# Kernel tuning notes

Measured on AMD Instinct MI355X. Metric: run time of the kernel, lower is better.

Reference implementation:

```python
import jax, jax.numpy as jnp
import numpy as np

B, C_IN, C_OUT, H, W, K, NK = 16, 256, 256, 64, 64, 3, 2
EPS = 1e-8


def setup_inputs() -> dict:
    key = jax.random.key(0)
    k1, k2, k3, k4 = jax.random.split(key, 4)
    x = jax.random.normal(k1, (B, C_IN, H, W), dtype=jnp.float32)
    mod = jax.random.normal(k2, (B, C_IN), dtype=jnp.float32)
    kernel_mod = jax.random.normal(k3, (B, NK), dtype=jnp.float32)
    # kernel bank: [num_conv_kernels, dim_out, dim_in, k, k] (kaiming-ish scale)
    weights = jax.random.normal(k4, (NK, C_OUT, C_IN, K, K), dtype=jnp.float32) / np.sqrt(C_IN * K * K)
    gamma = jnp.ones((C_OUT,), dtype=jnp.float32)
    return {"x": x, "mod": mod, "kernel_mod": kernel_mod, "weights": weights, "gamma": gamma}


def _block(x, mod, kernel_mod, weights, gamma):
    # adaptive kernel selection: softmax-mix the kernel bank per sample
    attn = jax.nn.softmax(kernel_mod, axis=-1)                       # [b, n]
    w = jnp.einsum('bn,noikl->boikl', attn, weights)                 # [b, o, i, k, k]
    # style modulation over input channels
    w = w * (mod[:, None, :, None, None] + 1.0)
    # demodulation
    denom = jnp.clip(jnp.sum(w * w, axis=(2, 3, 4), keepdims=True), EPS)
    w = w * jax.lax.rsqrt(denom)
    # per-sample conv (groups=b trick in torch) -> vmap over batch
    def conv_one(fmap, wb):
        return jax.lax.conv_general_dilated(
            fmap[None], wb, window_strides=(1, 1), padding='SAME',
            dimension_numbers=('NCHW', 'OIHW', 'NCHW'))[0]
    y = jax.vmap(conv_one)(x, w)                                     # [b, o, h, w]
    # RMSNorm over channel dim: F.normalize(x, dim=1) * gamma * sqrt(dim)
    norm = jnp.sqrt(jnp.sum(y * y, axis=1, keepdims=True))
    y = y / jnp.maximum(norm, 1e-12)
    y = y * gamma[None, :, None, None] * (gamma.shape[0] ** 0.5)
    # SiLU
    return y * jax.nn.sigmoid(y)


def reference(x, mod, kernel_mod, weights, gamma):
    return _block(x, mod, kernel_mod, weights, gamma)
```

## Files before the change

kernel.cpp:

```cpp
#include <hip/hip_runtime.h>
#include <math.h>


typedef __attribute__((ext_vector_type(8))) short short8;
typedef __attribute__((ext_vector_type(16))) float f32x16;

#define GLL16(src, dst)                                                       \
  __builtin_amdgcn_global_load_lds(                                           \
      (const __attribute__((address_space(1))) unsigned int*)(src),           \
      (__attribute__((address_space(3))) unsigned int*)(dst), 16, 0, 0)

static __device__ __forceinline__ unsigned short f2bf(float v) {
  union { float f; unsigned u; } u;
  u.f = v;
  unsigned r = u.u + 0x7FFF + ((u.u >> 16) & 1);
  return (unsigned short)(r >> 16);
}

__global__ __launch_bounds__(256) void wprep(
    const float* __restrict__ mod, const float* __restrict__ kmod,
    const float* __restrict__ weights, unsigned short* __restrict__ wq) {
  int blk = blockIdx.x;
  int b = blk >> 5, oq = blk & 31;
  int t = threadIdx.x;
  int o_l = t >> 5, its = t & 31;
  int o = oq * 8 + o_l;

  float k0 = kmod[b * 2 + 0], k1 = kmod[b * 2 + 1];
  float mx = fmaxf(k0, k1);
  float e0 = expf(k0 - mx), e1 = expf(k1 - mx);
  float ai = 1.0f / (e0 + e1);
  float a0 = e0 * ai, a1 = e1 * ai;

  float wv[9][8];
  float s = 0.0f;
  const float* w0 = &weights[((size_t)o * 256 + its * 8) * 9];
  const float* w1 = w0 + 589824;
#pragma unroll
  for (int e = 0; e < 8; ++e) {
    float f = mod[b * 256 + its * 8 + e] + 1.0f;
#pragma unroll
    for (int j = 0; j < 9; ++j) {
      float v = (a0 * w0[e * 9 + j] + a1 * w1[e * 9 + j]) * f;
      wv[j][e] = v;
      s = fmaf(v, v, s);
    }
  }

  __shared__ float red[8][32];
  __shared__ float scl[8];
  red[o_l][its] = s;
  __syncthreads();
  if (t < 8) {
    float tot = 0.0f;
#pragma unroll
    for (int k = 0; k < 32; ++k) tot += red[t][k];
    scl[t] = rsqrtf(fmaxf(tot, 1e-8f));
  }
  __syncthreads();
  float sc = scl[o_l];

  int c = its >> 1, io = its & 1;
  int oh = o >> 7, mf = (o >> 5) & 3;
  int lane2 = (o & 31) + io * 32;
  size_t cbase = ((size_t)(b * 16 + c)) * 36864 + oh * 2048 + mf * 512 + lane2 * 8;
#pragma unroll
  for (int j = 0; j < 9; ++j) {
    short8 pk;
#pragma unroll
    for (int e = 0; e < 8; ++e) pk[e] = (short)f2bf(wv[j][e] * sc);
    *(short8*)(wq + cbase + j * 4096) = pk;
  }
}

__global__ __launch_bounds__(256) void xprep(
    const float* __restrict__ x, unsigned short* __restrict__ xq) {
  int blk = blockIdx.x;
  int rowp = blk % 66;
  int bc = blk / 66;
  int b = bc >> 4, c = bc & 15;
  int t = threadIdx.x;
  size_t obase = (size_t)blk * 1056;

  if (rowp == 0 || rowp == 65) {
    for (int idx = t; idx < 1056; idx += 256) xq[obase + idx] = 0;
    return;
  }
  __shared__ __align__(16) unsigned short xs2[1056];
  int row = rowp - 1;
  for (int idx = t; idx < 1056; idx += 256) xs2[idx] = 0;
  __syncthreads();
#pragma unroll
  for (int k = 0; k < 4; ++k) {
    int idx = t + k * 256;
    int il = idx >> 6, col = idx & 63;
    float v = x[(((size_t)b * 256 + c * 16 + il) * 64 + row) * 64 + col];
    xs2[(col + 1) * 16 + il] = f2bf(v);
  }
  __syncthreads();
  if (t < 132) *(short8*)(xq + obase + (size_t)t * 8) = *(const short8*)&xs2[t * 8];
}

__global__ __launch_bounds__(512, 2) void conv_fused(
    const unsigned short* __restrict__ xq, const unsigned short* __restrict__ wq,
    const float* __restrict__ gamma, float* __restrict__ out) {
  __shared__ __align__(16) unsigned short xsm[2][8192];
  __shared__ float redl[1024];
  __shared__ float invs[256];
  __shared__ float gsm[256];

  int bid = blockIdx.x;
  int xcd = bid & 7;
  int kk = bid >> 3;
  int b = xcd * 2 + (kk >> 4);
  int rt = kk & 15;
  int r0 = rt * 4;

  int t = threadIdx.x;
  int w = t >> 6, lane = t & 63;
  int oh = w & 1, ps = w >> 1;
  int l31 = lane & 31, l5 = lane >> 5;

  if (t < 256) gsm[t] = gamma[t];

  int boffs[9];
#pragma unroll
  for (int T = 0; T < 9; ++T) {
    int kh = T / 3, kw = T % 3;
    boffs[T] = (ps + kh) * 2112 + (l31 + kw) * 32 + l5 * 16;
  }

  f32x16 acc[4][2];
#pragma unroll
  for (int mf = 0; mf < 4; ++mf)
#pragma unroll
    for (int h = 0; h < 2; ++h)
#pragma unroll
      for (int q = 0; q < 16; ++q) acc[mf][h][q] = 0.f;

#define GLLX(cn, nb)                                                           \
  _Pragma("unroll") for (int r = 0; r < 2; ++r) {                              \
    GLL16(xq + ((size_t)((b * 16 + (cn)) * 66 + r0)) * 1056 + (r * 512 + t) * 8, \
          &xsm[nb][(r * 512 + t) * 8]);                                        \
  }

#define AGLB(SA, CC, TT)                                                       \
  {                                                                            \
    const unsigned short* ap_ = wq + (size_t)(b * 16 + (CC)) * 36864 +         \
                                (TT) * 4096 + oh * 2048 + lane * 8;            \
    _Pragma("unroll") for (int mf = 0; mf < 4; ++mf)                           \
        SA[mf] = *(const short8*)(ap_ + mf * 512);                             \
  }

#define BDSRD(SB, T, XB)                                                       \
  {                                                                            \
    _Pragma("unroll") for (int h = 0; h < 2; ++h)                              \
        SB[h] = *(const short8*)((XB) + boffs[T] + h * 1024);                  \
  }

#define MFMA8(SA, SB)                                                          \
  {                                                                            \
    __builtin_amdgcn_s_setprio(1);                                             \
    _Pragma("unroll") for (int h = 0; h < 2; ++h)                              \
        _Pragma("unroll") for (int mf = 0; mf < 4; ++mf)                       \
            acc[mf][h] = __builtin_amdgcn_mfma_f32_32x32x16_bf16(              \
                SA[mf], SB[h], acc[mf][h], 0, 0, 0);                           \
    __builtin_amdgcn_s_setprio(0);                                             \
  }

#define SBAR __builtin_amdgcn_sched_barrier(0)
#define BAR __builtin_amdgcn_s_barrier()

  short8 PA[4], QA[4], PB[2], QB[2];

  const char* xs0 = (const char*)xsm[0];
  const char* xs1 = (const char*)xsm[1];

#define STEP(C, A0, A1, XB)                                                    \
  {                                                                            \
    int CN = (C) < 15 ? (C) + 1 : 15;                                          \
    GLLX(CN, ((C)&1) ^ 1);                                                     \
    BDSRD(PB, 0, XB); SBAR;                                                    \
    BDSRD(QB, 1, XB); SBAR; MFMA8(A0, PB); AGLB(A0, (C), 2); SBAR;             \
    BDSRD(PB, 2, XB); SBAR; MFMA8(A1, QB); AGLB(A1, (C), 3); SBAR;             \
    BDSRD(QB, 3, XB); SBAR; MFMA8(A0, PB); AGLB(A0, (C), 4); SBAR;             \
    BDSRD(PB, 4, XB); SBAR; MFMA8(A1, QB); AGLB(A1, (C), 5); SBAR;             \
    BDSRD(QB, 5, XB); SBAR; MFMA8(A0, PB); AGLB(A0, (C), 6); SBAR;             \
    BDSRD(PB, 6, XB); SBAR; MFMA8(A1, QB); AGLB(A1, (C), 7); SBAR;             \
    BDSRD(QB, 7, XB); SBAR; MFMA8(A0, PB); AGLB(A0, (C), 8); SBAR;             \
    BDSRD(PB, 8, XB); SBAR; MFMA8(A1, QB); AGLB(A1, CN, 0); SBAR;              \
    MFMA8(A0, PB); AGLB(A0, CN, 1); SBAR;                                      \
    asm volatile("s_waitcnt vmcnt(8) lgkmcnt(0)" ::: "memory");                \
    BAR;                                                                       \
    SBAR;                                                                      \
  }

  GLLX(0, 0);
  asm volatile("s_waitcnt vmcnt(0)" ::: "memory");
  BAR;
  SBAR;
  AGLB(PA, 0, 0);
  AGLB(QA, 0, 1);
  SBAR;

  for (int cc = 0; cc < 16; cc += 2) {
    STEP(cc, PA, QA, xs0);
    STEP(cc + 1, QA, PA, xs1);
  }

#pragma unroll
  for (int h = 0; h < 2; ++h) {
    float pssum = 0.f;
#pragma unroll
    for (int mf = 0; mf < 4; ++mf)
#pragma unroll
      for (int q = 0; q < 16; ++q) {
        float v = acc[mf][h][q];
        pssum = fmaf(v, v, pssum);
      }
    int px = ps * 64 + h * 32 + l31;
    redl[(oh * 2 + l5) * 256 + px] = pssum;
  }
  __syncthreads();
  if (t < 256) {
    float ssum = redl[t] + redl[256 + t] + redl[512 + t] + redl[768 + t];
    invs[t] = 16.0f / fmaxf(sqrtf(ssum), 1e-12f);
  }
  __syncthreads();
  float iv2[2];
#pragma unroll
  for (int h = 0; h < 2; ++h) iv2[h] = invs[ps * 64 + h * 32 + l31];

#pragma unroll
  for (int mf = 0; mf < 4; ++mf)
#pragma unroll
    for (int q = 0; q < 16; ++q) {
      int o = oh * 128 + mf * 32 + (q & 3) + 8 * (q >> 2) + 4 * l5;
      float g = gsm[o];
      size_t ob = ((size_t)b * 256 + o) * 64 + (r0 + ps);
#pragma unroll
      for (int h = 0; h < 2; ++h) {
        float v = acc[mf][h][q] * iv2[h] * g;
        float sg = 1.0f / (1.0f + expf(-v));
        out[ob * 64 + h * 32 + l31] = v * sg;
      }
    }
#undef GLLX
#undef AGLB
#undef BDSRD
#undef MFMA8
#undef SBAR
#undef BAR
#undef STEP
}

extern "C" void kernel_launch(void* const* d_in, const int* in_sizes, int n_in,
                              void* d_out, int out_size, void* d_ws, size_t ws_size,
                              hipStream_t stream) {
  const float* x = (const float*)d_in[0];
  const float* mod = (const float*)d_in[1];
  const float* kmod = (const float*)d_in[2];
  const float* weights = (const float*)d_in[3];
  const float* gamma = (const float*)d_in[4];
  float* out = (float*)d_out;

  unsigned short* xq = (unsigned short*)d_ws;
  unsigned short* wq = (unsigned short*)((char*)d_ws + 35684352);

  wprep<<<512, 256, 0, stream>>>(mod, kmod, weights, wq);
  xprep<<<16 * 16 * 66, 256, 0, stream>>>(x, xq);
  conv_fused<<<256, 512, 0, stream>>>(xq, wq, gamma, out);
}
```

Measured before the change: 124.5 us.

## Merge prep kernels and halve conv row tile to 256-thread blocks

Weight prep and input prep are merged into one launch, with block index ranges choosing the task, which removes a kernel launch and lets the two overlap. The conv kernel now handles 2 output rows per block with 4 waves instead of 4 rows with 8 waves, so the grid doubles to 512 blocks with smaller LDS buffers. The prologue now issues the first weight-fragment loads alongside the input tile load instead of after it. The trade-off is that each block re-reads the full per-sample weight set for half as many output pixels, roughly doubling weight traffic from L2.

Result: slower. 130.6 us (+4.9%).

```diff
diff --git a/kernel.cpp b/kernel.cpp
--- a/kernel.cpp
+++ b/kernel.cpp
@@ -17,111 +17,111 @@
   return (unsigned short)(r >> 16);
 }
 
-__global__ __launch_bounds__(256) void wprep(
-    const float* __restrict__ mod, const float* __restrict__ kmod,
-    const float* __restrict__ weights, unsigned short* __restrict__ wq) {
-  int blk = blockIdx.x;
-  int b = blk >> 5, oq = blk & 31;
-  int t = threadIdx.x;
-  int o_l = t >> 5, its = t & 31;
-  int o = oq * 8 + o_l;
-
-  float k0 = kmod[b * 2 + 0], k1 = kmod[b * 2 + 1];
-  float mx = fmaxf(k0, k1);
-  float e0 = expf(k0 - mx), e1 = expf(k1 - mx);
-  float ai = 1.0f / (e0 + e1);
-  float a0 = e0 * ai, a1 = e1 * ai;
-
-  float wv[9][8];
-  float s = 0.0f;
-  const float* w0 = &weights[((size_t)o * 256 + its * 8) * 9];
-  const float* w1 = w0 + 589824;
-#pragma unroll
-  for (int e = 0; e < 8; ++e) {
-    float f = mod[b * 256 + its * 8 + e] + 1.0f;
-#pragma unroll
-    for (int j = 0; j < 9; ++j) {
-      float v = (a0 * w0[e * 9 + j] + a1 * w1[e * 9 + j]) * f;
-      wv[j][e] = v;
-      s = fmaf(v, v, s);
-    }
-  }
-
+__global__ __launch_bounds__(256) void prep_all(
+    const float* __restrict__ x, const float* __restrict__ mod,
+    const float* __restrict__ kmod, const float* __restrict__ weights,
+    unsigned short* __restrict__ wq, unsigned short* __restrict__ xq) {
+  __shared__ __align__(16) unsigned short xs2[1056];
   __shared__ float red[8][32];
   __shared__ float scl[8];
-  red[o_l][its] = s;
-  __syncthreads();
-  if (t < 8) {
-    float tot = 0.0f;
-#pragma unroll
-    for (int k = 0; k < 32; ++k) tot += red[t][k];
-    scl[t] = rsqrtf(fmaxf(tot, 1e-8f));
-  }
-  __syncthreads();
-  float sc = scl[o_l];
-
-  int c = its >> 1, io = its & 1;
-  int oh = o >> 7, mf = (o >> 5) & 3;
-  int lane2 = (o & 31) + io * 32;
-  size_t cbase = ((size_t)(b * 16 + c)) * 36864 + oh * 2048 + mf * 512 + lane2 * 8;
-#pragma unroll
-  for (int j = 0; j < 9; ++j) {
-    short8 pk;
-#pragma unroll
-    for (int e = 0; e < 8; ++e) pk[e] = (short)f2bf(wv[j][e] * sc);
-    *(short8*)(wq + cbase + j * 4096) = pk;
-  }
-}
-
-__global__ __launch_bounds__(256) void xprep(
-    const float* __restrict__ x, unsigned short* __restrict__ xq) {
-  int blk = blockIdx.x;
-  int rowp = blk % 66;
-  int bc = blk / 66;
-  int b = bc >> 4, c = bc & 15;
   int t = threadIdx.x;
-  size_t obase = (size_t)blk * 1056;
-
-  if (rowp == 0 || rowp == 65) {
-    for (int idx = t; idx < 1056; idx += 256) xq[obase + idx] = 0;
-    return;
-  }
-  __shared__ __align__(16) unsigned short xs2[1056];
-  int row = rowp - 1;
-  for (int idx = t; idx < 1056; idx += 256) xs2[idx] = 0;
-  __syncthreads();
-#pragma unroll
-  for (int k = 0; k < 4; ++k) {
-    int idx = t + k * 256;
-    int il = idx >> 6, col = idx & 63;
-    float v = x[(((size_t)b * 256 + c * 16 + il) * 64 + row) * 64 + col];
-    xs2[(col + 1) * 16 + il] = f2bf(v);
-  }
-  __syncthreads();
-  if (t < 132) *(short8*)(xq + obase + (size_t)t * 8) = *(const short8*)&xs2[t * 8];
-}
-
-__global__ __launch_bounds__(512, 2) void conv_fused(
+
+  if (blockIdx.x < 16896) {
+    int blk = blockIdx.x;
+    int rowp = blk % 66;
+    int bc = blk / 66;
+    int b = bc >> 4, c = bc & 15;
+    size_t obase = (size_t)blk * 1056;
+
+    if (rowp == 0 || rowp == 65) {
+      for (int idx = t; idx < 1056; idx += 256) xq[obase + idx] = 0;
+      return;
+    }
+    int row = rowp - 1;
+    for (int idx = t; idx < 1056; idx += 256) xs2[idx] = 0;
+    __syncthreads();
+#pragma unroll
+    for (int k = 0; k < 4; ++k) {
+      int idx = t + k * 256;
+      int il = idx >> 6, col = idx & 63;
+      float v = x[(((size_t)b * 256 + c * 16 + il) * 64 + row) * 64 + col];
+      xs2[(col + 1) * 16 + il] = f2bf(v);
+    }
+    __syncthreads();
+    if (t < 132) *(short8*)(xq + obase + (size_t)t * 8) = *(const short8*)&xs2[t * 8];
+  } else {
+    int blk = blockIdx.x - 16896;
+    int b = blk >> 5, oq = blk & 31;
+    int o_l = t >> 5, its = t & 31;
+    int o = oq * 8 + o_l;
+
+    float k0 = kmod[b * 2 + 0], k1 = kmod[b * 2 + 1];
+    float mx = fmaxf(k0, k1);
+    float e0 = expf(k0 - mx), e1 = expf(k1 - mx);
+    float ai = 1.0f / (e0 + e1);
+    float a0 = e0 * ai, a1 = e1 * ai;
+
+    float wv[9][8];
+    float s = 0.0f;
+    const float* w0 = &weights[((size_t)o * 256 + its * 8) * 9];
+    const float* w1 = w0 + 589824;
+#pragma unroll
+    for (int e = 0; e < 8; ++e) {
+      float f = mod[b * 256 + its * 8 + e] + 1.0f;
+#pragma unroll
+      for (int j = 0; j < 9; ++j) {
+        float v = (a0 * w0[e * 9 + j] + a1 * w1[e * 9 + j]) * f;
+        wv[j][e] = v;
+        s = fmaf(v, v, s);
+      }
+    }
+
+    red[o_l][its] = s;
+    __syncthreads();
+    if (t < 8) {
+      float tot = 0.0f;
+#pragma unroll
+      for (int k = 0; k < 32; ++k) tot += red[t][k];
+      scl[t] = rsqrtf(fmaxf(tot, 1e-8f));
+    }
+    __syncthreads();
+    float sc = scl[o_l];
+
+    int c = its >> 1, io = its & 1;
+    int oh = o >> 7, mf = (o >> 5) & 3;
+    int lane2 = (o & 31) + io * 32;
+    size_t cbase = ((size_t)(b * 16 + c)) * 36864 + oh * 2048 + mf * 512 + lane2 * 8;
+#pragma unroll
+    for (int j = 0; j < 9; ++j) {
+      short8 pk;
+#pragma unroll
+      for (int e = 0; e < 8; ++e) pk[e] = (short)f2bf(wv[j][e] * sc);
+      *(short8*)(wq + cbase + j * 4096) = pk;
+    }
+  }
+}
+
+__global__ __launch_bounds__(256, 2) void conv_fused(
     const unsigned short* __restrict__ xq, const unsigned short* __restrict__ wq,
     const float* __restrict__ gamma, float* __restrict__ out) {
-  __shared__ __align__(16) unsigned short xsm[2][8192];
-  __shared__ float redl[1024];
-  __shared__ float invs[256];
+  __shared__ __align__(16) unsigned short xsm[2][6144];
+  __shared__ float redl[512];
+  __shared__ float invs[128];
   __shared__ float gsm[256];
 
   int bid = blockIdx.x;
   int xcd = bid & 7;
   int kk = bid >> 3;
-  int b = xcd * 2 + (kk >> 4);
-  int rt = kk & 15;
-  int r0 = rt * 4;
+  int b = xcd * 2 + (kk >> 5);
+  int rt = kk & 31;
+  int r0 = rt * 2;
 
   int t = threadIdx.x;
   int w = t >> 6, lane = t & 63;
   int oh = w & 1, ps = w >> 1;
   int l31 = lane & 31, l5 = lane >> 5;
 
-  if (t < 256) gsm[t] = gamma[t];
+  gsm[t] = gamma[t];
 
   int boffs[9];
 #pragma unroll
@@ -139,9 +139,9 @@
       for (int q = 0; q < 16; ++q) acc[mf][h][q] = 0.f;
 
 #define GLLX(cn, nb)                                                           \
-  _Pragma("unroll") for (int r = 0; r < 2; ++r) {                              \
-    GLL16(xq + ((size_t)((b * 16 + (cn)) * 66 + r0)) * 1056 + (r * 512 + t) * 8, \
-          &xsm[nb][(r * 512 + t) * 8]);                                        \
+  _Pragma("unroll") for (int r = 0; r < 3; ++r) {                              \
+    GLL16(xq + ((size_t)((b * 16 + (cn)) * 66 + r0)) * 1056 + (r * 256 + t) * 8, \
+          &xsm[nb][(r * 256 + t) * 8]);                                        \
   }
 
 #define AGLB(SA, CC, TT)                                                       \
@@ -169,6 +169,8 @@
   }
 
 #define SBAR __builtin_amdgcn_sched_barrier(0)
+#define LGKM0 asm volatile("s_waitcnt lgkmcnt(0)" ::: "memory")
+#define VMC(n) asm volatile("s_waitcnt vmcnt(" #n ")" ::: "memory")
 #define BAR __builtin_amdgcn_s_barrier()
 
   short8 PA[4], QA[4], PB[2], QB[2];
@@ -176,10 +178,10 @@
   const char* xs0 = (const char*)xsm[0];
   const char* xs1 = (const char*)xsm[1];
 
-#define STEP(C, A0, A1, XB)                                                    \
+#define STEP(C, A0, A1, XB, NB)                                                \
   {                                                                            \
     int CN = (C) < 15 ? (C) + 1 : 15;                                          \
-    GLLX(CN, ((C)&1) ^ 1);                                                     \
+    GLLX(CN, NB);                                                              \
     BDSRD(PB, 0, XB); SBAR;                                                    \
     BDSRD(QB, 1, XB); SBAR; MFMA8(A0, PB); AGLB(A0, (C), 2); SBAR;             \
     BDSRD(PB, 2, XB); SBAR; MFMA8(A1, QB); AGLB(A1, (C), 3); SBAR;             \
@@ -190,22 +192,22 @@
     BDSRD(QB, 7, XB); SBAR; MFMA8(A0, PB); AGLB(A0, (C), 8); SBAR;             \
     BDSRD(PB, 8, XB); SBAR; MFMA8(A1, QB); AGLB(A1, CN, 0); SBAR;              \
     MFMA8(A0, PB); AGLB(A0, CN, 1); SBAR;                                      \
-    asm volatile("s_waitcnt vmcnt(8) lgkmcnt(0)" ::: "memory");                \
+    LGKM0;                                                                     \
+    VMC(8);                                                                    \
     BAR;                                                                       \
     SBAR;                                                                      \
   }
 
   GLLX(0, 0);
-  asm volatile("s_waitcnt vmcnt(0)" ::: "memory");
+  AGLB(PA, 0, 0);
+  AGLB(QA, 0, 1);
+  VMC(8);
   BAR;
   SBAR;
-  AGLB(PA, 0, 0);
-  AGLB(QA, 0, 1);
-  SBAR;
 
   for (int cc = 0; cc < 16; cc += 2) {
-    STEP(cc, PA, QA, xs0);
-    STEP(cc + 1, QA, PA, xs1);
+    STEP(cc, PA, QA, xs0, 1);
+    STEP(cc + 1, QA, PA, xs1, 0);
   }
 
 #pragma unroll
@@ -219,11 +221,11 @@
         pssum = fmaf(v, v, pssum);
       }
     int px = ps * 64 + h * 32 + l31;
-    redl[(oh * 2 + l5) * 256 + px] = pssum;
+    redl[(oh * 2 + l5) * 128 + px] = pssum;
   }
   __syncthreads();
-  if (t < 256) {
-    float ssum = redl[t] + redl[256 + t] + redl[512 + t] + redl[768 + t];
+  if (t < 128) {
+    float ssum = redl[t] + redl[128 + t] + redl[256 + t] + redl[384 + t];
     invs[t] = 16.0f / fmaxf(sqrtf(ssum), 1e-12f);
   }
   __syncthreads();
@@ -250,6 +252,8 @@
 #undef BDSRD
 #undef MFMA8
 #undef SBAR
+#undef LGKM0
+#undef VMC
 #undef BAR
 #undef STEP
 }
@@ -267,7 +271,6 @@
   unsigned short* xq = (unsigned short*)d_ws;
   unsigned short* wq = (unsigned short*)((char*)d_ws + 35684352);
 
-  wprep<<<512, 256, 0, stream>>>(mod, kmod, weights, wq);
-  xprep<<<16 * 16 * 66, 256, 0, stream>>>(x, xq);
-  conv_fused<<<256, 512, 0, stream>>>(xq, wq, gamma, out);
-}
+  prep_all<<<16896 + 512, 256, 0, stream>>>(x, mod, kmod, weights, wq, xq);
+  conv_fused<<<512, 256, 0, stream>>>(xq, wq, gamma, out);
+}
```
